# Optimization experiments

Measured on AMD Instinct MI355X. Metric: run time of the kernel, lower is better.

## Reference

```python
import jax, jax.numpy as jnp
import numpy as np

PNS = (1, 2, 3, 4, 6, 8, 12, 16)
N_E, E_DIM = 8192, 256
BETA = 0.25
ALPHA = 0.5  # abs(quant_resi)
B, HW = 64, 16


def _area_mat(out_n, in_n):
    # torch adaptive_avg_pool1d matrix (F.interpolate mode='area')
    M = np.zeros((out_n, in_n), np.float32)
    for i in range(out_n):
        s = (i * in_n) // out_n
        e = -((-(i + 1) * in_n) // out_n)  # ceil((i+1)*in_n/out_n)
        M[i, s:e] = 1.0 / (e - s)
    return M


def _cubic_w(t):
    a = -0.75  # torch bicubic coefficient
    t = abs(t)
    if t <= 1.0:
        return (a + 2) * t ** 3 - (a + 3) * t ** 2 + 1.0
    if t < 2.0:
        return a * t ** 3 - 5 * a * t ** 2 + 8 * a * t - 4 * a
    return 0.0


def _bicubic_mat(out_n, in_n):
    # torch F.interpolate mode='bicubic', align_corners=False, border-replicate taps
    M = np.zeros((out_n, in_n), np.float32)
    scale = in_n / out_n
    for i in range(out_n):
        x = (i + 0.5) * scale - 0.5
        f = int(np.floor(x))
        for k in range(-1, 3):
            idx = min(max(f + k, 0), in_n - 1)
            M[i, idx] += _cubic_w(x - (f + k))
    return M


def setup_inputs() -> dict:
    key = jax.random.key(0)
    k1, k2, k3 = jax.random.split(key, 3)
    z = jax.random.normal(k1, (B, E_DIM, HW, HW), jnp.float32)
    embedding = jax.random.normal(k2, (N_E, E_DIM), jnp.float32)
    conv_w = jax.random.normal(k3, (len(PNS), E_DIM, E_DIM, 3, 3), jnp.float32) * 0.02
    conv_b = jnp.zeros((len(PNS), E_DIM), jnp.float32)
    return {"z": z, "embedding": embedding, "conv_w": conv_w, "conv_b": conv_b}


def reference(z, embedding, conv_w, conv_b):
    Bz, C, H, W = z.shape
    S = len(PNS)
    z_rest = z
    z_hat = jnp.zeros_like(z)
    total_loss = jnp.zeros((), z.dtype)
    counts = jnp.zeros((N_E,), z.dtype)
    e_sq = jnp.sum(embedding ** 2, axis=1)  # [n_e]
    for si, pn in enumerate(PNS):
        if si != S - 1:
            A = jnp.asarray(_area_mat(pn, H))
            zd = jnp.einsum('ph,qw,bchw->bpqc', A, A, z_rest)  # [B,pn,pn,C]
        else:
            zd = jnp.transpose(z_rest, (0, 2, 3, 1))
        zf = zd.reshape(-1, C)  # [N,C]
        dist = jnp.sum(zf ** 2, axis=1, keepdims=True) + e_sq - 2.0 * (zf @ embedding.T)
        idx = jnp.argmin(dist, axis=1)  # [N]
        zk = embedding[idx].reshape(zd.shape)  # [B,pn,pn,C]
        zk = jnp.transpose(zk, (0, 3, 1, 2))  # [B,C,pn,pn]
        if si != S - 1:
            U = jnp.asarray(_bicubic_mat(H, pn))
            zu = jnp.einsum('hp,wq,bcpq->bchw', U, U, zk)
        else:
            zu = zk
        y = jax.lax.conv_general_dilated(
            zu, conv_w[si], (1, 1), 'SAME',
            dimension_numbers=('NCHW', 'OIHW', 'NCHW')) + conv_b[si][None, :, None, None]
        res = zu * (1.0 - ALPHA) + y * ALPHA
        z_hat = z_hat + res
        z_rest = z_rest - res
        counts = counts.at[idx].add(jnp.asarray(1.0, z.dtype))
        total_loss = total_loss + BETA * jnp.mean((jax.lax.stop_gradient(z_hat) - z) ** 2)
    mean_vq_loss = total_loss / S
    z_hat_out = z + jax.lax.stop_gradient(z_hat - z)
    return z_hat_out, mean_vq_loss, counts
```

## Files before the change

### kernel.cpp

```cpp
#include <hip/hip_runtime.h>
#include <math.h>

#define NB 64
#define NC 256
#define NHW 16
#define NE 8192
#define NUMEL 4194304
#define LOSS_OFF 4194304
#define CNT_OFF  4194305

typedef __bf16 bf16x8 __attribute__((ext_vector_type(8)));
typedef float  f32x4  __attribute__((ext_vector_type(4)));

#define GLOAD_LDS(gptr, lptr) \
  __builtin_amdgcn_global_load_lds( \
      (const __attribute__((address_space(1))) unsigned int*)(gptr), \
      (__attribute__((address_space(3))) unsigned int*)(lptr), 16, 0, 0)

__device__ __forceinline__ float cubicw(float t) {
  t = fabsf(t);
  if (t <= 1.0f) return (1.25f * t - 2.25f) * t * t + 1.0f;
  if (t < 2.0f)  return ((-0.75f * t + 3.75f) * t - 6.0f) * t + 3.0f;
  return 0.0f;
}

__device__ __forceinline__ short f2bf(float x) {
  union { float f; unsigned int u; } v; v.f = x;
  unsigned int r = v.u + 0x7fffu + ((v.u >> 16) & 1u);
  return (short)(r >> 16);
}
__device__ __forceinline__ float bf2f(short h) {
  union { float f; unsigned int u; } v;
  v.u = ((unsigned int)(unsigned short)h) << 16;
  return v.f;
}

__global__ void k_zero(float* a, int na) {
  int i = blockIdx.x * 256 + threadIdx.x;
  if (i < na) a[i] = 0.0f;
}

__global__ void k_tr_in(const float* __restrict__ z, float* __restrict__ zrest) {
  int n = blockIdx.x, c = threadIdx.x;
  int b = n >> 8, hw = n & 255;
  zrest[(size_t)n * 256 + c] = z[((size_t)(b * 256 + c)) * 256 + hw];
}

__global__ void k_prep_emb2(const float* __restrict__ emb, short* __restrict__ B2,
                            float* __restrict__ esq) {
  int j = blockIdx.x, t = threadIdx.x;
  float v = emb[(size_t)j * 256 + t];
  short hi = f2bf(v);
  short lo = f2bf(v - bf2f(hi));
  B2[(size_t)j * 768 + t]       = hi;
  B2[(size_t)j * 768 + 256 + t] = hi;
  B2[(size_t)j * 768 + 512 + t] = lo;
  __shared__ float red[256];
  red[t] = v * v;
  __syncthreads();
  for (int s = 128; s > 0; s >>= 1) { if (t < s) red[t] += red[t + s]; __syncthreads(); }
  if (t == 0) esq[j] = red[0];
}

__global__ void k_prep_wb(const float* __restrict__ w, short* __restrict__ wB2) {
  int m = blockIdx.x * 256 + threadIdx.x;
  if (m >= 8 * 9 * 65536) return;
  int i = m & 255, o = (m >> 8) & 255;
  int r = m >> 16;
  int si = r / 9, tap = r % 9;
  float v = w[(((size_t)si * 256 + o) * 256 + i) * 9 + tap];
  short hi = f2bf(v);
  short lo = f2bf(v - bf2f(hi));
  size_t dst = ((size_t)r * 256 + o) * 768;
  wB2[dst + i]       = hi;
  wB2[dst + 256 + i] = hi;
  wB2[dst + 512 + i] = lo;
}

__global__ void k_down_a2(const float* __restrict__ zrest, short* __restrict__ A2, int pn) {
  int pq = blockIdx.x, b = blockIdx.y, c = threadIdx.x;
  int p = pq / pn, q = pq % pn;
  int sp = (p * 16) / pn, ep = ((p + 1) * 16 + pn - 1) / pn;
  int sq = (q * 16) / pn, eq = ((q + 1) * 16 + pn - 1) / pn;
  float s = 0.0f;
  for (int h = sp; h < ep; h++)
    for (int w = sq; w < eq; w++)
      s += zrest[((size_t)((b * 16 + h) * 16 + w)) * 256 + c];
  float x = s / (float)((ep - sp) * (eq - sq));
  int n = (b * pn + p) * pn + q;
  short hi = f2bf(x);
  short lo = f2bf(x - bf2f(hi));
  A2[(size_t)n * 768 + c]       = hi;
  A2[(size_t)n * 768 + 256 + c] = lo;
  A2[(size_t)n * 768 + 512 + c] = hi;
}

__global__ void k_split_a2(const float* __restrict__ zrest, short* __restrict__ A2) {
  int n = blockIdx.x, c = threadIdx.x;
  float x = zrest[(size_t)n * 256 + c];
  short hi = f2bf(x);
  short lo = f2bf(x - bf2f(hi));
  A2[(size_t)n * 768 + c]       = hi;
  A2[(size_t)n * 768 + 256 + c] = lo;
  A2[(size_t)n * 768 + 512 + c] = hi;
}

__global__ __launch_bounds__(512, 2) void k_dist_mfma(
    const short* __restrict__ A2, const short* __restrict__ B2,
    const float* __restrict__ esq, float* __restrict__ pd, int* __restrict__ pi,
    int N) {
  __shared__ short As[2][256 * 64];
  __shared__ short Bs[2][256 * 64];
  int t = threadIdx.x, ln = t & 63, wv = t >> 6;
  int wr = wv >> 2, wc = wv & 3;
  int n0 = blockIdx.x * 256;
  int jb0 = blockIdx.y * 256;
  int lc = ln & 15, lq = ln >> 4;

  f32x4 acc[8][4];
#pragma unroll
  for (int at = 0; at < 8; at++)
#pragma unroll
    for (int ac = 0; ac < 4; ac++) acc[at][ac] = (f32x4)(0.0f);

#pragma unroll
  for (int i = 0; i < 4; i++) {
    int Lb = i * 512 + wv * 64;
    int L = Lb + ln;
    int row = L >> 3, cc = L & 7;
    int gc = cc ^ (row & 7);
    GLOAD_LDS(A2 + (size_t)(n0 + row) * 768 + gc * 8, &As[0][Lb * 8]);
  }
#pragma unroll
  for (int i = 0; i < 4; i++) {
    int Lb = i * 512 + wv * 64;
    int L = Lb + ln;
    int row = L >> 3, cc = L & 7;
    int gc = cc ^ (row & 7);
    GLOAD_LDS(B2 + (size_t)(jb0 + row) * 768 + gc * 8, &Bs[0][Lb * 8]);
  }
  __syncthreads();

  for (int kt = 0; kt < 12; kt++) {
    int buf = kt & 1, nb = buf ^ 1;
    int kk2 = (kt + 1) * 64;

    bf16x8 fa03[2][4], fa47[2][4], fbA[2][2], fbB[2][2];

#pragma unroll
    for (int ks = 0; ks < 2; ks++) {
#pragma unroll
      for (int rt = 0; rt < 4; rt++) {
        int row = wr * 128 + rt * 16 + lc;
        int cc = (ks * 4 + lq) ^ (row & 7);
        fa03[ks][rt] = *(const bf16x8*)(&As[buf][row * 64 + cc * 8]);
      }
#pragma unroll
      for (int ct = 0; ct < 2; ct++) {
        int row = wc * 64 + ct * 16 + lc;
        int cc = (ks * 4 + lq) ^ (row & 7);
        fbA[ks][ct] = *(const bf16x8*)(&Bs[buf][row * 64 + cc * 8]);
      }
    }
    if (kt < 11) {
#pragma unroll
      for (int i = 0; i < 4; i++) {
        int Lb = i * 512 + wv * 64;
        int L = Lb + ln;
        int row = L >> 3, cc = L & 7;
        int gc = cc ^ (row & 7);
        GLOAD_LDS(A2 + (size_t)(n0 + row) * 768 + kk2 + gc * 8, &As[nb][Lb * 8]);
      }
    }
    __builtin_amdgcn_s_barrier();
    __builtin_amdgcn_s_setprio(1);
#pragma unroll
    for (int ks = 0; ks < 2; ks++)
#pragma unroll
      for (int rt = 0; rt < 4; rt++)
#pragma unroll
        for (int ct = 0; ct < 2; ct++)
          acc[rt][ct] = __builtin_amdgcn_mfma_f32_16x16x32_bf16(
              fa03[ks][rt], fbA[ks][ct], acc[rt][ct], 0, 0, 0);
    __builtin_amdgcn_s_setprio(0);
    __builtin_amdgcn_s_barrier();

#pragma unroll
    for (int ks = 0; ks < 2; ks++)
#pragma unroll
      for (int ct = 0; ct < 2; ct++) {
        int row = wc * 64 + 32 + ct * 16 + lc;
        int cc = (ks * 4 + lq) ^ (row & 7);
        fbB[ks][ct] = *(const bf16x8*)(&Bs[buf][row * 64 + cc * 8]);
      }
    if (kt < 11) {
#pragma unroll
      for (int i = 0; i < 4; i++) {
        int Lb = i * 512 + wv * 64;
        int L = Lb + ln;
        int row = L >> 3, cc = L & 7;
        int gc = cc ^ (row & 7);
        GLOAD_LDS(B2 + (size_t)(jb0 + row) * 768 + kk2 + gc * 8, &Bs[nb][Lb * 8]);
      }
    }
    __builtin_amdgcn_s_barrier();
    __builtin_amdgcn_s_setprio(1);
#pragma unroll
    for (int ks = 0; ks < 2; ks++)
#pragma unroll
      for (int rt = 0; rt < 4; rt++)
#pragma unroll
        for (int ct = 0; ct < 2; ct++)
          acc[rt][2 + ct] = __builtin_amdgcn_mfma_f32_16x16x32_bf16(
              fa03[ks][rt], fbB[ks][ct], acc[rt][2 + ct], 0, 0, 0);
    __builtin_amdgcn_s_setprio(0);
    __builtin_amdgcn_s_barrier();

#pragma unroll
    for (int ks = 0; ks < 2; ks++)
#pragma unroll
      for (int rt = 0; rt < 4; rt++) {
        int row = wr * 128 + 64 + rt * 16 + lc;
        int cc = (ks * 4 + lq) ^ (row & 7);
        fa47[ks][rt] = *(const bf16x8*)(&As[buf][row * 64 + cc * 8]);
      }
    __builtin_amdgcn_s_barrier();
    __builtin_amdgcn_s_setprio(1);
#pragma unroll
    for (int ks = 0; ks < 2; ks++)
#pragma unroll
      for (int rt = 0; rt < 4; rt++)
#pragma unroll
        for (int ct = 0; ct < 2; ct++)
          acc[4 + rt][2 + ct] = __builtin_amdgcn_mfma_f32_16x16x32_bf16(
              fa47[ks][rt], fbB[ks][ct], acc[4 + rt][2 + ct], 0, 0, 0);
    __builtin_amdgcn_s_setprio(0);
    __builtin_amdgcn_s_barrier();

    __builtin_amdgcn_s_setprio(1);
#pragma unroll
    for (int ks = 0; ks < 2; ks++)
#pragma unroll
      for (int rt = 0; rt < 4; rt++)
#pragma unroll
        for (int ct = 0; ct < 2; ct++)
          acc[4 + rt][ct] = __builtin_amdgcn_mfma_f32_16x16x32_bf16(
              fa47[ks][rt], fbA[ks][ct], acc[4 + rt][ct], 0, 0, 0);
    __builtin_amdgcn_s_setprio(0);

    __syncthreads();
  }

  float* sbd = (float*)(&As[0][0]);
  int*   sbi = (int*)((char*)(&As[0][0]) + 4096);

#pragma unroll
  for (int at = 0; at < 8; at++) {
    float bst[4]; int bix[4];
#pragma unroll
    for (int r = 0; r < 4; r++) { bst[r] = 3.4e38f; bix[r] = 0; }
#pragma unroll
    for (int ac = 0; ac < 4; ac++) {
      int j = jb0 + wc * 64 + ac * 16 + lc;
      float es = esq[j];
#pragma unroll
      for (int r = 0; r < 4; r++) {
        float d = es - 2.0f * acc[at][ac][r];
        if (d < bst[r]) { bst[r] = d; bix[r] = j; }
      }
    }
#pragma unroll
    for (int r = 0; r < 4; r++) {
      float bd = bst[r]; int bi = bix[r];
#pragma unroll
      for (int off = 1; off < 16; off <<= 1) {
        float od = __shfl_xor(bd, off, 64);
        int   oi = __shfl_xor(bi, off, 64);
        if (od < bd || (od == bd && oi < bi)) { bd = od; bi = oi; }
      }
      if (lc == 0) {
        int rl = wr * 128 + at * 16 + lq * 4 + r;
        sbd[wc * 256 + rl] = bd;
        sbi[wc * 256 + rl] = bi;
      }
    }
  }
  __syncthreads();
  if (t < 256) {
    float b0 = sbd[t]; int i0 = sbi[t];
#pragma unroll
    for (int w = 1; w < 4; w++) {
      float b1 = sbd[w * 256 + t]; int i1 = sbi[w * 256 + t];
      if (b1 < b0 || (b1 == b0 && i1 < i0)) { b0 = b1; i0 = i1; }
    }
    int n = n0 + t;
    if (n < N) {
      pd[(size_t)n * 32 + blockIdx.y] = b0;
      pi[(size_t)n * 32 + blockIdx.y] = i0;
    }
  }
}

__global__ void k_red(const float* __restrict__ pd, const int* __restrict__ pi,
                      int* __restrict__ idxb, float* __restrict__ counts, int N, int nct) {
  int n = blockIdx.x * 256 + threadIdx.x;
  if (n >= N) return;
  float bd = pd[(size_t)n * nct]; int bi = pi[(size_t)n * nct];
  for (int jt = 1; jt < nct; jt++) {
    float d = pd[(size_t)n * nct + jt]; int ii = pi[(size_t)n * nct + jt];
    if (d < bd || (d == bd && ii < bi)) { bd = d; bi = ii; }
  }
  idxb[n] = bi;
  atomicAdd(counts + bi, 1.0f);
}

__global__ void k_up(const float* __restrict__ emb, const int* __restrict__ idxb,
                     float* __restrict__ zu, short* __restrict__ zu2, int pn, int last) {
  int n = blockIdx.x, c = threadIdx.x;
  float acc;
  if (last) {
    acc = emb[(size_t)idxb[n] * 256 + c];
  } else {
    int b = n >> 8, hw = n & 255, h = hw >> 4, w = hw & 15;
    float scale = pn / 16.0f;
    float xh = (h + 0.5f) * scale - 0.5f; int fh = (int)floorf(xh);
    float xw = (w + 0.5f) * scale - 0.5f; int fw = (int)floorf(xw);
    int ph[4], pw[4]; float wh[4], wwt[4];
#pragma unroll
    for (int k = 0; k < 4; k++) {
      wh[k] = cubicw(xh - (float)(fh + k - 1));
      int pp = fh + k - 1; ph[k] = min(max(pp, 0), pn - 1);
      wwt[k] = cubicw(xw - (float)(fw + k - 1));
      pp = fw + k - 1; pw[k] = min(max(pp, 0), pn - 1);
    }
    acc = 0.0f;
#pragma unroll
    for (int kh = 0; kh < 4; kh++)
#pragma unroll
      for (int kw = 0; kw < 4; kw++) {
        int row = idxb[(n >> 8) * pn * pn + ph[kh] * pn + pw[kw]];
        acc += wh[kh] * wwt[kw] * emb[(size_t)row * 256 + c];
      }
  }
  zu[(size_t)n * 256 + c] = acc;
  short hi = f2bf(acc);
  short lo = f2bf(acc - bf2f(hi));
  zu2[(size_t)n * 768 + c]       = hi;
  zu2[(size_t)n * 768 + 256 + c] = lo;
  zu2[(size_t)n * 768 + 512 + c] = hi;
}

__global__ __launch_bounds__(512, 2) void k_conv_mfma(
    const short* __restrict__ zu2, const short* __restrict__ wB2,
    const float* __restrict__ cb, const float* __restrict__ zu,
    float* __restrict__ zrest, float* __restrict__ out_loss, int si) {
  __shared__ short Ah[2][108 * 64];
  __shared__ short Bs[2][256 * 64];
  __shared__ float red[512];
  int t = threadIdx.x, ln = t & 63, wv = t >> 6;
  int pxh = wv >> 2, oq = wv & 3;
  int lc = ln & 15, lq = ln >> 4;
  int b = blockIdx.x >> 2, h0 = (blockIdx.x & 3) * 4;

  bool awr[2], aval[2]; const short* asrc[2]; int adst[2];
#pragma unroll
  for (int i = 0; i < 2; i++) {
    int c = t * 2 + i;
    int rh = c >> 3, cc = c & 7;
    int hh = rh / 18, wx = rh - hh * 18;
    int h = h0 + hh - 1, w = wx - 1;
    awr[i]  = (c < 864);
    aval[i] = awr[i] && (h >= 0) && (h < 16) && (w >= 0) && (w < 16);
    int n = aval[i] ? (b * 256 + h * 16 + w) : 0;
    asrc[i] = zu2 + (size_t)n * 768 + cc * 8;
    adst[i] = rh * 64 + (cc ^ (rh & 7)) * 8;
  }

  f32x4 acc[2][4];
#pragma unroll
  for (int pf = 0; pf < 2; pf++)
#pragma unroll
    for (int ct = 0; ct < 4; ct++) acc[pf][ct] = (f32x4)(0.0f);

  {
    uint4 a0 = make_uint4(0u, 0u, 0u, 0u), a1 = make_uint4(0u, 0u, 0u, 0u);
    if (aval[0]) a0 = *(const uint4*)(asrc[0]);
    if (aval[1]) a1 = *(const uint4*)(asrc[1]);
    const short* bbase = wB2 + ((size_t)si * 9 * 256) * 768;
#pragma unroll
    for (int i = 0; i < 4; i++) {
      int Lb = i * 512 + wv * 64;
      int L = Lb + ln;
      int row = L >> 3, cc = L & 7;
      int gc = cc ^ (row & 7);
      GLOAD_LDS(bbase + (size_t)row * 768 + gc * 8, &Bs[0][Lb * 8]);
    }
    if (awr[0]) *(uint4*)(&Ah[0][adst[0]]) = a0;
    if (awr[1]) *(uint4*)(&Ah[0][adst[1]]) = a1;
  }
  __syncthreads();

  for (int kc = 0; kc < 12; kc++) {
    int ab = kc & 1;
    uint4 na0 = make_uint4(0u, 0u, 0u, 0u), na1 = make_uint4(0u, 0u, 0u, 0u);
#pragma unroll
    for (int tap = 0; tap < 9; tap++) {
      int dh = tap / 3 - 1, dw = tap % 3 - 1;
      int bbuf = (kc & 1) ^ (tap & 1);
      bf16x8 fa[2][2], fb[2][4];
#pragma unroll
      for (int ks = 0; ks < 2; ks++) {
#pragma unroll
        for (int pf = 0; pf < 2; pf++) {
          int rh = (pxh * 2 + pf + dh + 1) * 18 + lc + dw + 1;
          int cc = (ks * 4 + lq) ^ (rh & 7);
          fa[ks][pf] = *(const bf16x8*)(&Ah[ab][rh * 64 + cc * 8]);
        }
#pragma unroll
        for (int ct = 0; ct < 4; ct++) {
          int row = oq * 64 + ct * 16 + lc;
          int cc = (ks * 4 + lq) ^ (lc & 7);
          fb[ks][ct] = *(const bf16x8*)(&Bs[bbuf][row * 64 + cc * 8]);
        }
      }
      if (kc < 11 || tap < 8) {
        int nt = (tap == 8) ? 0 : tap + 1;
        int nk = (tap == 8) ? kc + 1 : kc;
        const short* bbase = wB2 + (((size_t)si * 9 + nt) * 256) * 768 + nk * 64;
#pragma unroll
        for (int i = 0; i < 4; i++) {
          int Lb = i * 512 + wv * 64;
          int L = Lb + ln;
          int row = L >> 3, cc = L & 7;
          int gc = cc ^ (row & 7);
          GLOAD_LDS(bbase + (size_t)row * 768 + gc * 8, &Bs[bbuf ^ 1][Lb * 8]);
        }
      }
      if (tap == 0 && kc < 11) {
        int koff = (kc + 1) * 64;
        if (aval[0]) na0 = *(const uint4*)(asrc[0] + koff);
        if (aval[1]) na1 = *(const uint4*)(asrc[1] + koff);
      }
      if (tap == 8 && kc < 11) {
        if (awr[0]) *(uint4*)(&Ah[ab ^ 1][adst[0]]) = na0;
        if (awr[1]) *(uint4*)(&Ah[ab ^ 1][adst[1]]) = na1;
      }
      __builtin_amdgcn_s_barrier();
      __builtin_amdgcn_s_setprio(1);
#pragma unroll
      for (int ks = 0; ks < 2; ks++)
#pragma unroll
        for (int pf = 0; pf < 2; pf++)
#pragma unroll
          for (int ct = 0; ct < 4; ct++)
            acc[pf][ct] = __builtin_amdgcn_mfma_f32_16x16x32_bf16(
                fa[ks][pf], fb[ks][ct], acc[pf][ct], 0, 0, 0);
      __builtin_amdgcn_s_setprio(0);
      __syncthreads();
    }
  }

  float lsum = 0.0f;
#pragma unroll
  for (int ct = 0; ct < 4; ct++) {
    int o = oq * 64 + ct * 16 + lc;
    float bias = cb[si * 256 + o];
#pragma unroll
    for (int pf = 0; pf < 2; pf++) {
      int n = b * 256 + (h0 + pxh * 2 + pf) * 16;
#pragma unroll
      for (int r = 0; r < 4; r++) {
        size_t m = (size_t)(n + lq * 4 + r) * 256 + o;
        float y = acc[pf][ct][r] + bias;
        float res = 0.5f * (zu[m] + y);
        float nv = zrest[m] - res;
        zrest[m] = nv;
        lsum += nv * nv;
      }
    }
  }
  red[t] = lsum;
  __syncthreads();
  for (int s = 256; s > 0; s >>= 1) { if (t < s) red[t] += red[t + s]; __syncthreads(); }
  if (t == 0) atomicAdd(out_loss, red[0] * (0.25f / (8.0f * 4194304.0f)));
}

__global__ void k_out(const float* __restrict__ z, const float* __restrict__ zrest,
                      float* __restrict__ out) {
  int n = blockIdx.x, c = threadIdx.x;
  int b = n >> 8, hw = n & 255;
  size_t m = ((size_t)(b * 256 + c)) * 256 + hw;
  out[m] = z[m] - zrest[(size_t)n * 256 + c];
}

extern "C" void kernel_launch(void* const* d_in, const int* in_sizes, int n_in,
                              void* d_out, int out_size, void* d_ws, size_t ws_size,
                              hipStream_t stream) {
  const float* z   = (const float*)d_in[0];
  const float* emb = (const float*)d_in[1];
  const float* cw  = (const float*)d_in[2];
  const float* cb  = (const float*)d_in[3];
  float* out = (float*)d_out;
  float* ws  = (float*)d_ws;

  float* z_rest = ws;
  float* zu     = ws + 4194304;
  float* esq    = ws + 8388608;
  short* A2     = (short*)(ws + 8396800);
  short* zu2    = A2;
  short* B2     = (short*)(ws + 14688256);
  short* wB2    = (short*)(ws + 17833984);
  float* pd     = ws + 24911872;
  int*   pi     = (int*)(ws + 25436160);
  int*   idxb   = (int*)(ws + 25960448);

  const int pns[8] = {1, 2, 3, 4, 6, 8, 12, 16};

  k_zero<<<33, 256, 0, stream>>>(out + LOSS_OFF, 1 + NE);
  k_tr_in<<<16384, 256, 0, stream>>>(z, z_rest);
  k_prep_emb2<<<8192, 256, 0, stream>>>(emb, B2, esq);
  k_prep_wb<<<18432, 256, 0, stream>>>(cw, wB2);

  for (int si = 0; si < 8; si++) {
    int pn = pns[si];
    int N = 64 * pn * pn;
    if (si < 7)
      k_down_a2<<<dim3(pn * pn, 64), 256, 0, stream>>>(z_rest, A2, pn);
    else
      k_split_a2<<<16384, 256, 0, stream>>>(z_rest, A2);
    int rb = (N + 255) / 256;
    k_dist_mfma<<<dim3(rb, 32), 512, 0, stream>>>(A2, B2, esq, pd, pi, N);
    k_red<<<(N + 255) / 256, 256, 0, stream>>>(pd, pi, idxb, out + CNT_OFF, N, 32);
    k_up<<<16384, 256, 0, stream>>>(emb, idxb, zu, zu2, pn, si == 7 ? 1 : 0);
    k_conv_mfma<<<dim3(256), 512, 0, stream>>>(zu2, wB2, cb, zu, z_rest,
                                               out + LOSS_OFF, si);
  }
  k_out<<<16384, 256, 0, stream>>>(z, z_rest, out);
}
```

Before: 2.060 ms.

## Deepen LDS prefetch pipelines in distance and conv MFMA kernels with vmcnt waits

Result: no change. 2.053 ms (-0.3%).

```diff
diff --git a/kernel.cpp b/kernel.cpp
--- a/kernel.cpp
+++ b/kernel.cpp
@@ -109,8 +109,8 @@
     const short* __restrict__ A2, const short* __restrict__ B2,
     const float* __restrict__ esq, float* __restrict__ pd, int* __restrict__ pi,
     int N) {
-  __shared__ short As[2][256 * 64];
-  __shared__ short Bs[2][256 * 64];
+  __shared__ short As[4][256 * 32];
+  __shared__ short Bs[4][256 * 32];
   int t = threadIdx.x, ln = t & 63, wv = t >> 6;
   int wr = wv >> 2, wc = wv & 3;
   int n0 = blockIdx.x * 256;
@@ -123,133 +123,86 @@
 #pragma unroll
     for (int ac = 0; ac < 4; ac++) acc[at][ac] = (f32x4)(0.0f);
 
-#pragma unroll
-  for (int i = 0; i < 4; i++) {
-    int Lb = i * 512 + wv * 64;
-    int L = Lb + ln;
-    int row = L >> 3, cc = L & 7;
-    int gc = cc ^ (row & 7);
-    GLOAD_LDS(A2 + (size_t)(n0 + row) * 768 + gc * 8, &As[0][Lb * 8]);
-  }
-#pragma unroll
-  for (int i = 0; i < 4; i++) {
-    int Lb = i * 512 + wv * 64;
-    int L = Lb + ln;
-    int row = L >> 3, cc = L & 7;
-    int gc = cc ^ (row & 7);
-    GLOAD_LDS(B2 + (size_t)(jb0 + row) * 768 + gc * 8, &Bs[0][Lb * 8]);
-  }
-  __syncthreads();
-
-  for (int kt = 0; kt < 12; kt++) {
-    int buf = kt & 1, nb = buf ^ 1;
-    int kk2 = (kt + 1) * 64;
-
-    bf16x8 fa03[2][4], fa47[2][4], fbA[2][2], fbB[2][2];
-
-#pragma unroll
-    for (int ks = 0; ks < 2; ks++) {
-#pragma unroll
-      for (int rt = 0; rt < 4; rt++) {
-        int row = wr * 128 + rt * 16 + lc;
-        int cc = (ks * 4 + lq) ^ (row & 7);
-        fa03[ks][rt] = *(const bf16x8*)(&As[buf][row * 64 + cc * 8]);
-      }
-#pragma unroll
-      for (int ct = 0; ct < 2; ct++) {
-        int row = wc * 64 + ct * 16 + lc;
-        int cc = (ks * 4 + lq) ^ (row & 7);
-        fbA[ks][ct] = *(const bf16x8*)(&Bs[buf][row * 64 + cc * 8]);
-      }
-    }
-    if (kt < 11) {
-#pragma unroll
-      for (int i = 0; i < 4; i++) {
-        int Lb = i * 512 + wv * 64;
-        int L = Lb + ln;
-        int row = L >> 3, cc = L & 7;
-        int gc = cc ^ (row & 7);
-        GLOAD_LDS(A2 + (size_t)(n0 + row) * 768 + kk2 + gc * 8, &As[nb][Lb * 8]);
-      }
-    }
+#define DSTAGE(tile_, bsel_)                                                \
+  {                                                                         \
+    int kkS = (tile_) * 32;                                                 \
+    _Pragma("unroll")                                                       \
+    for (int i = 0; i < 2; i++) {                                           \
+      int Lb = i * 512 + wv * 64;                                           \
+      int L = Lb + ln;                                                      \
+      int row = L >> 2, cc = L & 3;                                         \
+      int gc = cc ^ (row & 3);                                              \
+      GLOAD_LDS(A2 + (size_t)(n0 + row) * 768 + kkS + gc * 8,               \
+                &As[(bsel_)][Lb * 8]);                                      \
+    }                                                                       \
+    _Pragma("unroll")                                                       \
+    for (int i = 0; i < 2; i++) {                                           \
+      int Lb = i * 512 + wv * 64;                                           \
+      int L = Lb + ln;                                                      \
+      int row = L >> 2, cc = L & 3;                                         \
+      int gc = cc ^ (row & 3);                                              \
+      GLOAD_LDS(B2 + (size_t)(jb0 + row) * 768 + kkS + gc * 8,              \
+                &Bs[(bsel_)][Lb * 8]);                                      \
+    }                                                                       \
+  }
+
+  DSTAGE(0, 0);
+  DSTAGE(1, 1);
+  DSTAGE(2, 2);
+  asm volatile("s_waitcnt vmcnt(8)" ::: "memory");
+  __builtin_amdgcn_s_barrier();
+
+#pragma unroll
+  for (int kt = 0; kt < 24; kt++) {
+    const int bsel = kt & 3;
+    bf16x8 fa0[4], fb[4];
+#pragma unroll
+    for (int rt = 0; rt < 4; rt++) {
+      int row = wr * 128 + rt * 16 + lc;
+      int cc = lq ^ (row & 3);
+      fa0[rt] = *(const bf16x8*)(&As[bsel][row * 32 + cc * 8]);
+    }
+#pragma unroll
+    for (int ct = 0; ct < 4; ct++) {
+      int row = wc * 64 + ct * 16 + lc;
+      int cc = lq ^ (row & 3);
+      fb[ct] = *(const bf16x8*)(&Bs[bsel][row * 32 + cc * 8]);
+    }
+    if (kt < 21) DSTAGE(kt + 3, (kt + 3) & 3);
     __builtin_amdgcn_s_barrier();
     __builtin_amdgcn_s_setprio(1);
 #pragma unroll
-    for (int ks = 0; ks < 2; ks++)
-#pragma unroll
-      for (int rt = 0; rt < 4; rt++)
-#pragma unroll
-        for (int ct = 0; ct < 2; ct++)
-          acc[rt][ct] = __builtin_amdgcn_mfma_f32_16x16x32_bf16(
-              fa03[ks][rt], fbA[ks][ct], acc[rt][ct], 0, 0, 0);
+    for (int rt = 0; rt < 4; rt++)
+#pragma unroll
+      for (int ct = 0; ct < 4; ct++)
+        acc[rt][ct] = __builtin_amdgcn_mfma_f32_16x16x32_bf16(
+            fa0[rt], fb[ct], acc[rt][ct], 0, 0, 0);
     __builtin_amdgcn_s_setprio(0);
     __builtin_amdgcn_s_barrier();
-
-#pragma unroll
-    for (int ks = 0; ks < 2; ks++)
-#pragma unroll
-      for (int ct = 0; ct < 2; ct++) {
-        int row = wc * 64 + 32 + ct * 16 + lc;
-        int cc = (ks * 4 + lq) ^ (row & 7);
-        fbB[ks][ct] = *(const bf16x8*)(&Bs[buf][row * 64 + cc * 8]);
-      }
-    if (kt < 11) {
-#pragma unroll
-      for (int i = 0; i < 4; i++) {
-        int Lb = i * 512 + wv * 64;
-        int L = Lb + ln;
-        int row = L >> 3, cc = L & 7;
-        int gc = cc ^ (row & 7);
-        GLOAD_LDS(B2 + (size_t)(jb0 + row) * 768 + kk2 + gc * 8, &Bs[nb][Lb * 8]);
-      }
+    bf16x8 fa1[4];
+#pragma unroll
+    for (int rt = 0; rt < 4; rt++) {
+      int row = wr * 128 + 64 + rt * 16 + lc;
+      int cc = lq ^ (row & 3);
+      fa1[rt] = *(const bf16x8*)(&As[bsel][row * 32 + cc * 8]);
     }
     __builtin_amdgcn_s_barrier();
     __builtin_amdgcn_s_setprio(1);
 #pragma unroll
-    for (int ks = 0; ks < 2; ks++)
-#pragma unroll
-      for (int rt = 0; rt < 4; rt++)
-#pragma unroll
-        for (int ct = 0; ct < 2; ct++)
-          acc[rt][2 + ct] = __builtin_amdgcn_mfma_f32_16x16x32_bf16(
-              fa03[ks][rt], fbB[ks][ct], acc[rt][2 + ct], 0, 0, 0);
+    for (int rt = 0; rt < 4; rt++)
+#pragma unroll
+      for (int ct = 0; ct < 4; ct++)
+        acc[4 + rt][ct] = __builtin_amdgcn_mfma_f32_16x16x32_bf16(
+            fa1[rt], fb[ct], acc[4 + rt][ct], 0, 0, 0);
     __builtin_amdgcn_s_setprio(0);
-    __builtin_amdgcn_s_barrier();
-
-#pragma unroll
-    for (int ks = 0; ks < 2; ks++)
-#pragma unroll
-      for (int rt = 0; rt < 4; rt++) {
-        int row = wr * 128 + 64 + rt * 16 + lc;
-        int cc = (ks * 4 + lq) ^ (row & 7);
-        fa47[ks][rt] = *(const bf16x8*)(&As[buf][row * 64 + cc * 8]);
-      }
-    __builtin_amdgcn_s_barrier();
-    __builtin_amdgcn_s_setprio(1);
-#pragma unroll
-    for (int ks = 0; ks < 2; ks++)
-#pragma unroll
-      for (int rt = 0; rt < 4; rt++)
-#pragma unroll
-        for (int ct = 0; ct < 2; ct++)
-          acc[4 + rt][2 + ct] = __builtin_amdgcn_mfma_f32_16x16x32_bf16(
-              fa47[ks][rt], fbB[ks][ct], acc[4 + rt][2 + ct], 0, 0, 0);
-    __builtin_amdgcn_s_setprio(0);
-    __builtin_amdgcn_s_barrier();
-
-    __builtin_amdgcn_s_setprio(1);
-#pragma unroll
-    for (int ks = 0; ks < 2; ks++)
-#pragma unroll
-      for (int rt = 0; rt < 4; rt++)
-#pragma unroll
-        for (int ct = 0; ct < 2; ct++)
-          acc[4 + rt][ct] = __builtin_amdgcn_mfma_f32_16x16x32_bf16(
-              fa47[ks][rt], fbA[ks][ct], acc[4 + rt][ct], 0, 0, 0);
-    __builtin_amdgcn_s_setprio(0);
-
-    __syncthreads();
-  }
+    if (kt < 23) {
+      if (kt < 21)       { asm volatile("s_waitcnt vmcnt(8)" ::: "memory"); }
+      else if (kt == 21) { asm volatile("s_waitcnt vmcnt(4)" ::: "memory"); }
+      else               { asm volatile("s_waitcnt vmcnt(0)" ::: "memory"); }
+      __builtin_amdgcn_s_barrier();
+    }
+  }
+#undef DSTAGE
 
   float* sbd = (float*)(&As[0][0]);
   int*   sbi = (int*)((char*)(&As[0][0]) + 4096);
@@ -355,7 +308,7 @@
     const float* __restrict__ cb, const float* __restrict__ zu,
     float* __restrict__ zrest, float* __restrict__ out_loss, int si) {
   __shared__ short Ah[2][108 * 64];
-  __shared__ short Bs[2][256 * 64];
+  __shared__ short Bs[3][256 * 64];
   __shared__ float red[512];
   int t = threadIdx.x, ln = t & 63, wv = t >> 6;
   int pxh = wv >> 2, oq = wv & 3;
@@ -376,6 +329,20 @@
     adst[i] = rh * 64 + (cc ^ (rh & 7)) * 8;
   }
 
+#define CSTAGE(nt_, nk_, bsel_)                                             \
+  {                                                                         \
+    const short* bbase =                                                    \
+        wB2 + (((size_t)si * 9 + (nt_)) * 256) * 768 + (nk_) * 64;          \
+    _Pragma("unroll")                                                       \
+    for (int i = 0; i < 4; i++) {                                           \
+      int Lb = i * 512 + wv * 64;                                           \
+      int L = Lb + ln;                                                      \
+      int row = L >> 3, cc = L & 7;                                         \
+      int gc = cc ^ (row & 7);                                              \
+      GLOAD_LDS(bbase + (size_t)row * 768 + gc * 8, &Bs[(bsel_)][Lb * 8]);  \
+    }                                                                       \
+  }
+
   f32x4 acc[2][4];
 #pragma unroll
   for (int pf = 0; pf < 2; pf++)
@@ -383,30 +350,25 @@
     for (int ct = 0; ct < 4; ct++) acc[pf][ct] = (f32x4)(0.0f);
 
   {
+    CSTAGE(0, 0, 0);
+    CSTAGE(1, 0, 1);
     uint4 a0 = make_uint4(0u, 0u, 0u, 0u), a1 = make_uint4(0u, 0u, 0u, 0u);
     if (aval[0]) a0 = *(const uint4*)(asrc[0]);
     if (aval[1]) a1 = *(const uint4*)(asrc[1]);
-    const short* bbase = wB2 + ((size_t)si * 9 * 256) * 768;
-#pragma unroll
-    for (int i = 0; i < 4; i++) {
-      int Lb = i * 512 + wv * 64;
-      int L = Lb + ln;
-      int row = L >> 3, cc = L & 7;
-      int gc = cc ^ (row & 7);
-      GLOAD_LDS(bbase + (size_t)row * 768 + gc * 8, &Bs[0][Lb * 8]);
-    }
     if (awr[0]) *(uint4*)(&Ah[0][adst[0]]) = a0;
     if (awr[1]) *(uint4*)(&Ah[0][adst[1]]) = a1;
-  }
-  __syncthreads();
+    asm volatile("s_waitcnt vmcnt(4) lgkmcnt(0)" ::: "memory");
+  }
+  __builtin_amdgcn_s_barrier();
 
   for (int kc = 0; kc < 12; kc++) {
     int ab = kc & 1;
     uint4 na0 = make_uint4(0u, 0u, 0u, 0u), na1 = make_uint4(0u, 0u, 0u, 0u);
 #pragma unroll
     for (int tap = 0; tap < 9; tap++) {
+      const int rb3 = tap % 3;
+      const int sb3 = (tap + 2) % 3;
       int dh = tap / 3 - 1, dw = tap % 3 - 1;
-      int bbuf = (kc & 1) ^ (tap & 1);
       bf16x8 fa[2][2], fb[2][4];
 #pragma unroll
       for (int ks = 0; ks < 2; ks++) {
@@ -420,21 +382,13 @@
         for (int ct = 0; ct < 4; ct++) {
           int row = oq * 64 + ct * 16 + lc;
           int cc = (ks * 4 + lq) ^ (lc & 7);
-          fb[ks][ct] = *(const bf16x8*)(&Bs[bbuf][row * 64 + cc * 8]);
+          fb[ks][ct] = *(const bf16x8*)(&Bs[rb3][row * 64 + cc * 8]);
         }
       }
-      if (kc < 11 || tap < 8) {
-        int nt = (tap == 8) ? 0 : tap + 1;
-        int nk = (tap == 8) ? kc + 1 : kc;
-        const short* bbase = wB2 + (((size_t)si * 9 + nt) * 256) * 768 + nk * 64;
-#pragma unroll
-        for (int i = 0; i < 4; i++) {
-          int Lb = i * 512 + wv * 64;
-          int L = Lb + ln;
-          int row = L >> 3, cc = L & 7;
-          int gc = cc ^ (row & 7);
-          GLOAD_LDS(bbase + (size_t)row * 768 + gc * 8, &Bs[bbuf ^ 1][Lb * 8]);
-        }
+      if (kc < 11 || tap < 7) {
+        int nt = (tap < 7) ? tap + 2 : tap - 7;
+        int nk = (tap < 7) ? kc : kc + 1;
+        CSTAGE(nt, nk, sb3);
       }
       if (tap == 0 && kc < 11) {
         int koff = (kc + 1) * 64;
@@ -456,9 +410,23 @@
             acc[pf][ct] = __builtin_amdgcn_mfma_f32_16x16x32_bf16(
                 fa[ks][pf], fb[ks][ct], acc[pf][ct], 0, 0, 0);
       __builtin_amdgcn_s_setprio(0);
-      __syncthreads();
-    }
-  }
+      if (tap == 8) {
+        if (kc < 11) {
+          asm volatile("s_waitcnt vmcnt(4) lgkmcnt(0)" ::: "memory");
+          __builtin_amdgcn_s_barrier();
+        }
+      } else if (tap == 7) {
+        if (kc < 11) { asm volatile("s_waitcnt vmcnt(4)" ::: "memory"); }
+        else         { asm volatile("s_waitcnt vmcnt(0)" ::: "memory"); }
+        __builtin_amdgcn_s_barrier();
+      } else {
+        asm volatile("s_waitcnt vmcnt(4)" ::: "memory");
+        __builtin_amdgcn_s_barrier();
+      }
+    }
+  }
+#undef CSTAGE
+  __syncthreads();
 
   float lsum = 0.0f;
 #pragma unroll
```
